# Optimization experiments

Measured on AMD Instinct MI355X. Metric: run time of the kernel, lower is better.

Reference implementation:

```python
import jax, jax.numpy as jnp
import numpy as np

N = 25000      # nodes
E = 300000     # edges
IN = 32        # in_dim
EDF = 16       # edge_feat_dim
HID = 256      # hidden_dim (per-head dim, concat=False)
HEADS = 4
ACT = 16       # num_actions
G = 64         # graphs in batch
KW = 1024      # wire-mask query nodes


def setup_inputs() -> dict:
    key = jax.random.key(0)
    ks = jax.random.split(key, 20)
    def rn(k, shape, s=0.1):
        return jax.random.normal(k, shape, jnp.float32) * s
    return {
        "x": jax.random.normal(ks[0], (N, IN), jnp.float32),
        "edge_attr": jax.random.normal(ks[1], (E, EDF), jnp.float32),
        "wire_mask": jax.random.randint(ks[2], (KW,), 0, N, jnp.int32),
        "edge_index": jax.random.randint(ks[3], (2, E), 0, N, jnp.int32),
        "batch": jnp.sort(jax.random.randint(ks[4], (N,), 0, G, jnp.int32)),
        "enc_w1": rn(ks[5], (EDF, 32)),
        "enc_b1": jnp.zeros((32,), jnp.float32),
        "enc_w2": rn(ks[6], (32, IN * IN), 0.05),
        "enc_b2": jnp.zeros((IN * IN,), jnp.float32),
        "root_w": rn(ks[7], (IN, IN)),
        "nn_bias": jnp.zeros((IN,), jnp.float32),
        "gat1_w": rn(ks[8], (IN, HEADS * HID)),
        "gat1_asrc": rn(ks[9], (HEADS, HID)),
        "gat1_adst": rn(ks[10], (HEADS, HID)),
        "gat1_b": jnp.zeros((HID,), jnp.float32),
        "gat2_w": rn(ks[11], (HID, HEADS * HID)),
        "gat2_asrc": rn(ks[12], (HEADS, HID)),
        "gat2_adst": rn(ks[13], (HEADS, HID)),
        "gat2_b": jnp.zeros((HID,), jnp.float32),
        "wire_w": rn(ks[14], (HID, 1)),
        "wire_b": jnp.zeros((1,), jnp.float32),
        "act_w": rn(ks[15], (HID, ACT)),
        "act_b": jnp.zeros((ACT,), jnp.float32),
    }


def _gat(x, src, dst, W, a_src, a_dst, b):
    # PyG GATConv, concat=False (mean over heads), eval mode (no dropout),
    # self-loops already included in (src, dst).
    H, D = a_src.shape
    h = (x @ W).reshape(-1, H, D)                      # [N, H, D]
    es = (h * a_src[None]).sum(-1)                     # [N, H]
    ed = (h * a_dst[None]).sum(-1)                     # [N, H]
    e = jax.nn.leaky_relu(es[src] + ed[dst], negative_slope=0.2)  # [E2, H]
    m = jax.ops.segment_max(e, dst, num_segments=N)    # segment softmax (stable)
    w = jnp.exp(e - m[dst])
    den = jax.ops.segment_sum(w, dst, num_segments=N)
    alpha = w / (den[dst] + 1e-16)
    out = jax.ops.segment_sum(h[src] * alpha[..., None], dst, num_segments=N)
    return out.mean(axis=1) + b                        # [N, D]


def reference(x, edge_attr, wire_mask, edge_index, batch,
              enc_w1, enc_b1, enc_w2, enc_b2, root_w, nn_bias,
              gat1_w, gat1_asrc, gat1_adst, gat1_b,
              gat2_w, gat2_asrc, gat2_adst, gat2_b,
              wire_w, wire_b, act_w, act_b):
    src, dst = edge_index[0], edge_index[1]
    # NNConv (aggr='mean'): per-edge weight matrix from edge MLP
    We = (jax.nn.relu(edge_attr @ enc_w1 + enc_b1) @ enc_w2 + enc_b2)
    We = We.reshape(E, IN, IN)                         # [E, in, out]
    msg = jnp.einsum('ei,eio->eo', x[src], We)         # [E, out]
    s = jax.ops.segment_sum(msg, dst, num_segments=N)
    cnt = jax.ops.segment_sum(jnp.ones((E,), x.dtype), dst, num_segments=N)
    agg = s / jnp.maximum(cnt, 1.0)[:, None]
    h0 = jax.nn.relu(agg + x @ root_w + nn_bias)
    # GATConv default add_self_loops=True
    sl = jnp.arange(N, dtype=src.dtype)
    src2 = jnp.concatenate([src, sl])
    dst2 = jnp.concatenate([dst, sl])
    h1 = jax.nn.relu(_gat(h0, src2, dst2, gat1_w, gat1_asrc, gat1_adst, gat1_b))
    h2 = jax.nn.relu(_gat(h1, src2, dst2, gat2_w, gat2_asrc, gat2_adst, gat2_b))
    p_wire = (h2[wire_mask] @ wire_w + wire_b).squeeze(-1)   # [KW]
    pooled_s = jax.ops.segment_sum(h2, batch, num_segments=G)
    gc = jax.ops.segment_sum(jnp.ones((N,), h2.dtype), batch, num_segments=G)
    pooled = pooled_s / jnp.maximum(gc, 1.0)[:, None]        # global_mean_pool
    p_action = pooled @ act_w + act_b                        # [G, ACT]
    return (p_wire, p_action)
```

## Files before the change

### kernel.cpp

```cpp
#include <hip/hip_runtime.h>
#include <hip/hip_fp16.h>

#define N_NODES 25000
#define M_PAD   25024
#define N_TILES 1564
#define N_EDGES 300000
#define IN_DIM  32
#define EDFD    16
#define HIDD    256
#define HEADS   4
#define NACT    16
#define NGRAPH  64
#define KWIRE   1024
#define POOL_NB 64

typedef _Float16 half8v __attribute__((ext_vector_type(8)));
typedef __attribute__((ext_vector_type(4))) float f32x4;

__device__ __forceinline__ float leaky(float v) { return v > 0.f ? v : 0.2f * v; }

__global__ __launch_bounds__(256) void k_deg2(const int* __restrict__ ei,
                                              int* __restrict__ deg,
                                              int* __restrict__ deg2) {
    int e = blockIdx.x * 256 + threadIdx.x;
    if (e >= N_EDGES) return;
    atomicAdd(&deg[ei[N_EDGES + e]], 1);
    atomicAdd(&deg2[ei[e]], 1);
}

__global__ __launch_bounds__(256) void k_scan2(const int* __restrict__ degA, int* __restrict__ rpA,
                                               const int* __restrict__ degB, int* __restrict__ rpB) {
    const int* deg = blockIdx.x ? degB : degA;
    int* rowptr    = blockIdx.x ? rpB : rpA;
    __shared__ int part[256];
    int t = threadIdx.x;
    const int CH = 98;
    int base = t * CH;
    int s = 0;
    for (int i = 0; i < CH; ++i) {
        int idx = base + i;
        if (idx < N_NODES) s += deg[idx];
    }
    part[t] = s;
    __syncthreads();
    if (t == 0) {
        int run = 0;
        for (int i = 0; i < 256; ++i) { int v = part[i]; part[i] = run; run += v; }
    }
    __syncthreads();
    int run = part[t];
    for (int i = 0; i < CH; ++i) {
        int idx = base + i;
        if (idx < N_NODES) { rowptr[idx] = run; run += deg[idx]; }
    }
    if (N_NODES >= base && N_NODES < base + CH) rowptr[N_NODES] = run;
}

__global__ __launch_bounds__(256) void k_scatter2(const int* __restrict__ ei,
                                                  const float* __restrict__ ea,
                                                  const int* __restrict__ rowptr,
                                                  const int* __restrict__ rowptr2,
                                                  int* __restrict__ cursor,
                                                  int* __restrict__ cursor2,
                                                  int* __restrict__ csrc,
                                                  int* __restrict__ cdst,
                                                  int* __restrict__ posMap,
                                                  __half* __restrict__ eaP) {
    int e = blockIdx.x * 256 + threadIdx.x;
    if (e >= N_EDGES) return;
    int src = ei[e], dst = ei[N_EDGES + e];
    int p1 = atomicAdd(&cursor[dst], 1);
    int r1 = rowptr[dst] + p1;
    csrc[r1] = src;
    int p2 = atomicAdd(&cursor2[src], 1);
    int r2 = rowptr2[src] + p2;
    cdst[r2] = dst;
    posMap[r2] = r1;
    const float4* src4 = (const float4*)(ea + (size_t)e * EDFD);
    __half2* dp = (__half2*)(eaP + (size_t)r2 * EDFD);
    #pragma unroll
    for (int q = 0; q < EDFD / 4; ++q) {
        float4 v = src4[q];
        dp[q * 2]     = __float22half2_rn(make_float2(v.x, v.y));
        dp[q * 2 + 1] = __float22half2_rn(make_float2(v.z, v.w));
    }
}

__global__ __launch_bounds__(256) void k_prep(const float* __restrict__ w2,
                                              const float* __restrict__ W1,
                                              const float* __restrict__ W2,
                                              const float* __restrict__ a1s,
                                              const float* __restrict__ a1d,
                                              const float* __restrict__ a2s,
                                              const float* __restrict__ a2d,
                                              const float* __restrict__ x,
                                              const float* __restrict__ b2,
                                              __half* __restrict__ wtt,
                                              __half* __restrict__ wb1,
                                              __half* __restrict__ wb2,
                                              float* __restrict__ wa1,
                                              float* __restrict__ wd1,
                                              float* __restrict__ wa2,
                                              float* __restrict__ wd2,
                                              __half* __restrict__ xf,
                                              float* __restrict__ xb) {
    int bid = blockIdx.x, t = threadIdx.x;
    if (bid < 128) {
        int idx = bid * 256 + t;
        int co = idx >> 5, i = idx & 31;
        wtt[idx] = __float2half(w2[(co >> 5) * 1024 + i * 32 + (co & 31)]);
    } else if (bid < 256) {
        int idx = (bid - 128) * 256 + t;
        int d = idx >> 7, k = idx & 127;
        int h = k >> 5, i = k & 31;
        wb1[idx] = __float2half(0.25f * W1[i * 1024 + h * 256 + d]);
    } else if (bid < 1280) {
        int idx = (bid - 256) * 256 + t;
        int d = idx >> 10, k = idx & 1023;
        int h = k >> 8, i = k & 255;
        wb2[idx] = __float2half(0.25f * W2[i * 1024 + h * 256 + d]);
    } else if (bid < 4405) {
        int idx = (bid - 1280) * 256 + t;
        if (idx >= N_NODES * 32) return;
        int n = idx >> 5, o = idx & 31;
        xf[idx] = __float2half(x[idx]);
        float s = 0.f;
        for (int i = 0; i < 32; ++i) s += x[n * 32 + i] * b2[i * 32 + o];
        xb[idx] = s;
    } else if (bid == 4405) {
        if (t >= 128) return;
        int h = t >> 5, i = t & 31;
        float s = 0.f, sd = 0.f;
        for (int d = 0; d < 256; ++d) {
            float w = W1[i * 1024 + h * 256 + d];
            s  += w * a1s[h * 256 + d];
            sd += w * a1d[h * 256 + d];
        }
        wa1[t] = s; wd1[t] = sd;
    } else {
        int idx = (bid - 4406) * 256 + t;
        if (idx >= 1024) return;
        int h = idx >> 8, i = idx & 255;
        float s = 0.f, sd = 0.f;
        for (int d = 0; d < 256; ++d) {
            float w = W2[i * 1024 + h * 256 + d];
            s  += w * a2s[h * 256 + d];
            sd += w * a2d[h * 256 + d];
        }
        wa2[idx] = s; wd2[idx] = sd;
    }
}

__global__ __launch_bounds__(256) void k_msg2(const int* __restrict__ rowptr2,
                                              const int* __restrict__ posMap,
                                              const __half* __restrict__ eaP,
                                              const float* __restrict__ w1,
                                              const float* __restrict__ b1,
                                              const __half* __restrict__ T,
                                              const float* __restrict__ xb,
                                              __half* __restrict__ msgE) {
    int g = threadIdx.x >> 5, o = threadIdx.x & 31;
    int src = blockIdx.x * 8 + g;
    if (src >= N_NODES) return;
    int r0 = rowptr2[src], r1 = rowptr2[src + 1];
    if (r0 == r1) return;
    float tcol[32];
    const __half* Tp = T + (size_t)src * 1024 + o;
    #pragma unroll
    for (int j = 0; j < 32; ++j) tcol[j] = __half2float(Tp[j * 32]);
    float w1col[EDFD];
    #pragma unroll
    for (int k = 0; k < EDFD; ++k) w1col[k] = w1[k * 32 + o];
    float b1o = b1[o];
    float xbv = xb[src * 32 + o];
    for (int r = r0; r < r1; ++r) {
        int pm = posMap[r];
        const __half2* h2p = (const __half2*)(eaP + (size_t)r * EDFD);
        float a = b1o;
        #pragma unroll
        for (int q = 0; q < EDFD / 2; ++q) {
            float2 v = __half22float2(h2p[q]);
            a += v.x * w1col[2 * q] + v.y * w1col[2 * q + 1];
        }
        a = fmaxf(a, 0.f);
        float m0 = 0.f, m1 = 0.f, m2 = 0.f, m3 = 0.f;
        #pragma unroll
        for (int j = 0; j < 32; j += 4) {
            m0 += __shfl(a, j,     32) * tcol[j];
            m1 += __shfl(a, j + 1, 32) * tcol[j + 1];
            m2 += __shfl(a, j + 2, 32) * tcol[j + 2];
            m3 += __shfl(a, j + 3, 32) * tcol[j + 3];
        }
        float m = xbv + ((m0 + m1) + (m2 + m3));
        msgE[(size_t)pm * 32 + o] = __float2half(m);
    }
}

__global__ __launch_bounds__(256) void k_h0e(const float* __restrict__ x,
                                             const float* __restrict__ root_w,
                                             const float* __restrict__ nn_bias,
                                             const __half* __restrict__ msgE,
                                             const int* __restrict__ rowptr,
                                             const float* __restrict__ wa,
                                             const float* __restrict__ wd,
                                             __half* __restrict__ h0f,
                                             float* __restrict__ es,
                                             float* __restrict__ ed) {
    int t = threadIdx.x;
    int ng = t >> 5, o = t & 31;
    int n = blockIdx.x * 8 + ng;
    if (n >= N_NODES) return;
    float s = nn_bias[o];
    for (int k = 0; k < IN_DIM; ++k) s += x[n * IN_DIM + k] * root_w[k * 32 + o];
    int r0 = rowptr[n], r1 = rowptr[n + 1];
    float aggv = 0.f;
    for (int r = r0; r < r1; ++r)
        aggv += __half2float(msgE[(size_t)r * 32 + o]);
    float c = fmaxf((float)(r1 - r0), 1.f);
    s += aggv / c;
    float v = fmaxf(s, 0.f);
    h0f[n * IN_DIM + o] = __float2half(v);
    #pragma unroll
    for (int h = 0; h < 4; ++h) {
        float ss = v * wa[h * 32 + o];
        float dd = v * wd[h * 32 + o];
        #pragma unroll
        for (int off = 16; off; off >>= 1) {
            ss += __shfl_down(ss, off, 32);
            dd += __shfl_down(dd, off, 32);
        }
        if (o == 0) { es[n * 4 + h] = ss; ed[n * 4 + h] = dd; }
    }
}

__global__ __launch_bounds__(256, 2) void k_gemT(const __half* __restrict__ A,
                                                 const __half* __restrict__ Wt,
                                                 __half* __restrict__ C) {
    __shared__ __half cst[4][16 * 36];
    int t = threadIdx.x, wid = t >> 6, lane = t & 63;
    int lr = lane & 15, lk = (lane >> 4) * 8;

    int bid = blockIdx.x;
    int xcd = bid & 7, j = bid >> 3;
    int sx = j & 31;
    int y = ((j >> 5) << 3) | xcd;
    int n0 = sx * 32;

    half8v bfr[2];
    #pragma unroll
    for (int c = 0; c < 2; ++c)
        bfr[c] = *(const half8v*)(Wt + (size_t)(n0 + c * 16 + lr) * 32 + lk);

    int tb = (y * 4 + wid) * 4;
    for (int pp = 0; pp < 4; pp += 2) {
        int tA = tb + pp;
        if (tA >= N_TILES) break;
        int mA = tA * 16, mB = mA + 16;
        half8v aA = *(const half8v*)(A + (size_t)(mA + lr) * 32 + lk);
        half8v aB = *(const half8v*)(A + (size_t)(mB + lr) * 32 + lk);
        f32x4 acc[2][2];
        #pragma unroll
        for (int i = 0; i < 2; ++i)
            #pragma unroll
            for (int c = 0; c < 2; ++c)
                acc[i][c] = (f32x4){0.f, 0.f, 0.f, 0.f};
        acc[0][0] = __builtin_amdgcn_mfma_f32_16x16x32_f16(aA, bfr[0], acc[0][0], 0, 0, 0);
        acc[0][1] = __builtin_amdgcn_mfma_f32_16x16x32_f16(aA, bfr[1], acc[0][1], 0, 0, 0);
        acc[1][0] = __builtin_amdgcn_mfma_f32_16x16x32_f16(aB, bfr[0], acc[1][0], 0, 0, 0);
        acc[1][1] = __builtin_amdgcn_mfma_f32_16x16x32_f16(aB, bfr[1], acc[1][1], 0, 0, 0);

        int rbase = (lane >> 4) * 4;
        #pragma unroll
        for (int ti = 0; ti < 2; ++ti) {
            #pragma unroll
            for (int c = 0; c < 2; ++c)
                #pragma unroll
                for (int r = 0; r < 4; ++r)
                    cst[wid][(rbase + r) * 36 + c * 16 + lr] = __float2half(acc[ti][c][r]);
            int m0 = ti ? mB : mA;
            #pragma unroll
            for (int p = 0; p < 2; ++p) {
                int row = p * 8 + (lane >> 3), hb = lane & 7;
                float2 v = *(const float2*)((const char*)&cst[wid][0] + row * 72 + hb * 8);
                *(float2*)((char*)C + ((size_t)(m0 + row) * 1024 + n0) * 2 + hb * 8) = v;
            }
        }
    }
}

template <int K, typename OT>
__global__ __launch_bounds__(256) void k_gemmo(const __half* __restrict__ A,
                                               const __half* __restrict__ Wt,
                                               const float* __restrict__ bias,
                                               OT* __restrict__ C) {
    constexpr int CK  = 128;
    constexpr int KC  = K / CK;
    constexpr int KSC = CK / 32;
    constexpr int CB  = CK * 2;
    __shared__ __half bs[2][32 * CK];
    __shared__ float cst[4][16 * 36];
    int t = threadIdx.x, wid = t >> 6, lane = t & 63;
    int lr = lane & 15, lk = (lane >> 4) * 8;

    int bid = blockIdx.x;
    int xcd = bid & 7, rest = bid >> 3;
    int strip = rest & 7, yhi = rest >> 3;
    int y = yhi * 8 + xcd;
    if (y >= 98) return;
    int n0 = strip * 32;
    float bv0 = bias[n0 + lr], bv1 = bias[n0 + 16 + lr];
    int tb = (y * 4 + wid) * 4;
    const int swz = (lr & 7) << 4;

    f32x4 acc[2][2][2];
    #pragma unroll
    for (int pi = 0; pi < 2; ++pi)
        #pragma unroll
        for (int i = 0; i < 2; ++i)
            #pragma unroll
            for (int c = 0; c < 2; ++c)
                acc[pi][i][c] = (f32x4){0.f, 0.f, 0.f, 0.f};

    for (int i = t * 16; i < 32 * CB; i += 256 * 16) {
        int col = i / CB, offb = i % CB;
        const char* src = (const char*)Wt + ((size_t)(n0 + col) * K) * 2 + offb;
        *(float4*)((char*)bs[0] + (i ^ ((col & 7) << 4))) = *(const float4*)src;
    }
    __syncthreads();

    for (int kc = 0; kc < KC; ++kc) {
        int cur = kc & 1;
        if (kc + 1 < KC) {
            for (int i = t * 16; i < 32 * CB; i += 256 * 16) {
                int col = i / CB, offb = i % CB;
                const char* src = (const char*)Wt + (((size_t)(n0 + col) * K + (kc + 1) * CK) * 2 + offb);
                *(float4*)((char*)bs[cur ^ 1] + (i ^ ((col & 7) << 4))) = *(const float4*)src;
            }
        }
        #pragma unroll
        for (int pi = 0; pi < 2; ++pi) {
            int tA = tb + pi * 2;
            if (tA >= N_TILES) continue;
            int mA = tA * 16, mB = mA + 16;
            const __half* pA = A + (size_t)(mA + lr) * K + kc * CK + lk;
            const __half* pB = A + (size_t)(mB + lr) * K + kc * CK + lk;
            #pragma unroll
            for (int ks = 0; ks < KSC; ++ks) {
                half8v aA = *(const half8v*)(pA + (size_t)ks * 32);
                half8v aB = *(const half8v*)(pB + (size_t)ks * 32);
                half8v b0 = *(const half8v*)((const char*)bs[cur] + ((( 0 + lr) * CB + lk * 2 + ks * 64) ^ swz));
                half8v b1 = *(const half8v*)((const char*)bs[cur] + (((16 + lr) * CB + lk * 2 + ks * 64) ^ swz));
                acc[pi][0][0] = __builtin_amdgcn_mfma_f32_16x16x32_f16(aA, b0, acc[pi][0][0], 0, 0, 0);
                acc[pi][0][1] = __builtin_amdgcn_mfma_f32_16x16x32_f16(aA, b1, acc[pi][0][1], 0, 0, 0);
                acc[pi][1][0] = __builtin_amdgcn_mfma_f32_16x16x32_f16(aB, b0, acc[pi][1][0], 0, 0, 0);
                acc[pi][1][1] = __builtin_amdgcn_mfma_f32_16x16x32_f16(aB, b1, acc[pi][1][1], 0, 0, 0);
            }
        }
        if (kc + 1 < KC) __syncthreads();
    }

    int rbase = (lane >> 4) * 4;
    #pragma unroll
    for (int pi = 0; pi < 2; ++pi) {
        int tA = tb + pi * 2;
        if (tA >= N_TILES) continue;
        #pragma unroll
        for (int ti = 0; ti < 2; ++ti) {
            #pragma unroll
            for (int c = 0; c < 2; ++c)
                #pragma unroll
                for (int r = 0; r < 4; ++r)
                    cst[wid][(rbase + r) * 36 + c * 16 + lr] =
                        fmaxf(acc[pi][ti][c][r] + (c ? bv1 : bv0), 0.f);
            int m0 = tA * 16 + ti * 16;
            int row = lane >> 2, cg = lane & 3;
            const float* sp = &cst[wid][row * 36 + cg * 8];
            if constexpr (sizeof(OT) == 2) {
                __half2 o0 = __float22half2_rn(make_float2(sp[0], sp[1]));
                __half2 o1 = __float22half2_rn(make_float2(sp[2], sp[3]));
                __half2 o2 = __float22half2_rn(make_float2(sp[4], sp[5]));
                __half2 o3 = __float22half2_rn(make_float2(sp[6], sp[7]));
                float4 v = make_float4(__uint_as_float(*(unsigned*)&o0), __uint_as_float(*(unsigned*)&o1),
                                       __uint_as_float(*(unsigned*)&o2), __uint_as_float(*(unsigned*)&o3));
                *(float4*)((__half*)C + (size_t)(m0 + row) * 256 + n0 + cg * 8) = v;
            } else {
                float4 v0 = make_float4(sp[0], sp[1], sp[2], sp[3]);
                float4 v1 = make_float4(sp[4], sp[5], sp[6], sp[7]);
                float* cp = (float*)C + (size_t)(m0 + row) * 256 + n0 + cg * 8;
                *(float4*)cp = v0;
                *(float4*)(cp + 4) = v1;
            }
        }
    }
}

__global__ __launch_bounds__(256) void k_esed2(const __half* __restrict__ h1f,
                                               const float* __restrict__ wa,
                                               const float* __restrict__ wd,
                                               float* __restrict__ es,
                                               float* __restrict__ ed) {
    int n = blockIdx.x;
    int h = threadIdx.x >> 6, lane = threadIdx.x & 63;
    float s = 0.f, d2 = 0.f;
    for (int d = lane; d < 256; d += 64) {
        float v = __half2float(h1f[(size_t)n * 256 + d]);
        s  += v * wa[h * 256 + d];
        d2 += v * wd[h * 256 + d];
    }
    #pragma unroll
    for (int off = 32; off; off >>= 1) {
        s  += __shfl_down(s, off);
        d2 += __shfl_down(d2, off);
    }
    if (lane == 0) { es[n * 4 + h] = s; ed[n * 4 + h] = d2; }
}

__global__ __launch_bounds__(256) void k_agg1(const int* __restrict__ rowptr,
                                              const int* __restrict__ csrc,
                                              const float* __restrict__ es,
                                              const float* __restrict__ ed,
                                              const __half* __restrict__ h0f,
                                              __half* __restrict__ agg0) {
    int dst = blockIdx.x * 4 + (threadIdx.x >> 6);
    if (dst >= N_NODES) return;
    int lane = threadIdx.x & 63;
    int h = lane >> 4, i2 = lane & 15;
    float edv = ed[dst * 4 + h];
    float vself = leaky(es[dst * 4 + h] + edv);
    float dn = 1.f;
    int r0 = rowptr[dst], r1 = rowptr[dst + 1];

    __half2 hv = *(const __half2*)(h0f + (size_t)dst * 32 + i2 * 2);
    float2 f = __half22float2(hv);
    float ax = f.x, ay = f.y;
    for (int r = r0; r < r1; ++r) {
        int src = csrc[r];
        float w = __expf(leaky(es[src * 4 + h] + edv) - vself);
        dn += w;
        __half2 sv = *(const __half2*)(h0f + (size_t)src * 32 + i2 * 2);
        float2 g = __half22float2(sv);
        ax += w * g.x; ay += w * g.y;
    }
    float inv = 1.f / (dn + 1e-16f);
    *(__half2*)(agg0 + (size_t)dst * 128 + h * 32 + i2 * 2) =
        __float22half2_rn(make_float2(ax * inv, ay * inv));
}

__global__ __launch_bounds__(256) void k_agg2(const int* __restrict__ rowptr,
                                              const int* __restrict__ csrc,
                                              const float* __restrict__ es,
                                              const float* __restrict__ ed,
                                              const __half* __restrict__ h1f,
                                              __half* __restrict__ agg1) {
    int dst = blockIdx.x * 4 + (threadIdx.x >> 6);
    if (dst >= N_NODES) return;
    int lane = threadIdx.x & 63;
    float vs[4], edv[4], dn[4];
    float acc[4][4];
    {
        float2 q = *(const float2*)(h1f + (size_t)dst * 256 + lane * 4);
        const __half2* hq = (const __half2*)&q;
        float2 f0 = __half22float2(hq[0]), f1 = __half22float2(hq[1]);
        #pragma unroll
        for (int h = 0; h < 4; ++h) {
            edv[h] = ed[dst * 4 + h];
            vs[h] = leaky(es[dst * 4 + h] + edv[h]);
            dn[h] = 1.f;
            acc[h][0] = f0.x; acc[h][1] = f0.y;
            acc[h][2] = f1.x; acc[h][3] = f1.y;
        }
    }
    int r0 = rowptr[dst], r1 = rowptr[dst + 1];
    for (int r = r0; r < r1; ++r) {
        int src = csrc[r];
        float4 esv = *(const float4*)(es + (size_t)src * 4);
        float w0 = __expf(leaky(esv.x + edv[0]) - vs[0]);
        float w1 = __expf(leaky(esv.y + edv[1]) - vs[1]);
        float w2 = __expf(leaky(esv.z + edv[2]) - vs[2]);
        float w3 = __expf(leaky(esv.w + edv[3]) - vs[3]);
        dn[0] += w0; dn[1] += w1; dn[2] += w2; dn[3] += w3;
        float2 q = *(const float2*)(h1f + (size_t)src * 256 + lane * 4);
        const __half2* hq = (const __half2*)&q;
        float2 f0 = __half22float2(hq[0]), f1 = __half22float2(hq[1]);
        acc[0][0] += w0 * f0.x; acc[0][1] += w0 * f0.y; acc[0][2] += w0 * f1.x; acc[0][3] += w0 * f1.y;
        acc[1][0] += w1 * f0.x; acc[1][1] += w1 * f0.y; acc[1][2] += w1 * f1.x; acc[1][3] += w1 * f1.y;
        acc[2][0] += w2 * f0.x; acc[2][1] += w2 * f0.y; acc[2][2] += w2 * f1.x; acc[2][3] += w2 * f1.y;
        acc[3][0] += w3 * f0.x; acc[3][1] += w3 * f0.y; acc[3][2] += w3 * f1.x; acc[3][3] += w3 * f1.y;
    }
    #pragma unroll
    for (int h = 0; h < 4; ++h) {
        float inv = 1.f / (dn[h] + 1e-16f);
        __half2 o0 = __float22half2_rn(make_float2(acc[h][0] * inv, acc[h][1] * inv));
        __half2 o1 = __float22half2_rn(make_float2(acc[h][2] * inv, acc[h][3] * inv));
        __half2* op = (__half2*)(agg1 + (size_t)dst * 1024 + h * 256 + lane * 4);
        op[0] = o0; op[1] = o1;
    }
}

__global__ __launch_bounds__(256) void k_wirepool(const int* __restrict__ wm,
                                                  const float* __restrict__ h2,
                                                  const float* __restrict__ ww,
                                                  const float* __restrict__ wb,
                                                  const int* __restrict__ batch,
                                                  float* __restrict__ out,
                                                  float* __restrict__ pooled,
                                                  float* __restrict__ gcnt) {
    int bid = blockIdx.x;
    if (bid < KWIRE / 4) {
        int k = bid * 4 + (threadIdx.x >> 6);
        int lane = threadIdx.x & 63;
        int n = wm[k];
        float s = 0.f;
        for (int d = lane; d < 256; d += 64) s += h2[(size_t)n * 256 + d] * ww[d];
        #pragma unroll
        for (int off = 32; off; off >>= 1) s += __shfl_down(s, off);
        if (lane == 0) out[k] = s + wb[0];
        return;
    }
    int n0 = (bid - KWIRE / 4) * POOL_NB;
    int n1 = n0 + POOL_NB; if (n1 > N_NODES) n1 = N_NODES;
    int d = threadIdx.x;
    int cur = batch[n0];
    float acc = 0.f, cnt = 0.f;
    for (int n = n0; n < n1; ++n) {
        int g = batch[n];
        if (g != cur) {
            atomicAdd(&pooled[cur * 256 + d], acc);
            if (d == 0) atomicAdd(&gcnt[cur], cnt);
            acc = 0.f; cnt = 0.f; cur = g;
        }
        acc += h2[(size_t)n * 256 + d];
        cnt += 1.f;
    }
    atomicAdd(&pooled[cur * 256 + d], acc);
    if (d == 0) atomicAdd(&gcnt[cur], cnt);
}

__global__ __launch_bounds__(256) void k_act(const float* __restrict__ pooled,
                                             const float* __restrict__ gcnt,
                                             const float* __restrict__ aw,
                                             const float* __restrict__ ab,
                                             float* __restrict__ out) {
    int u = blockIdx.x * 4 + (threadIdx.x >> 6);
    int lane = threadIdx.x & 63;
    if (u >= NGRAPH * NACT) return;
    int g = u >> 4, a = u & 15;
    float c = fmaxf(gcnt[g], 1.f);
    float s = 0.f;
    for (int d = lane; d < 256; d += 64) s += pooled[g * 256 + d] * aw[d * 16 + a];
    #pragma unroll
    for (int off = 32; off; off >>= 1) s += __shfl_down(s, off);
    if (lane == 0) out[KWIRE + u] = s / c + ab[a];
}

extern "C" void kernel_launch(void* const* d_in, const int* in_sizes, int n_in,
                              void* d_out, int out_size, void* d_ws, size_t ws_size,
                              hipStream_t stream) {
    const float* x        = (const float*)d_in[0];
    const float* edge_attr= (const float*)d_in[1];
    const int*   wire_mask= (const int*)d_in[2];
    const int*   edge_idx = (const int*)d_in[3];
    const int*   batch    = (const int*)d_in[4];
    const float* enc_w1   = (const float*)d_in[5];
    const float* enc_b1   = (const float*)d_in[6];
    const float* enc_w2   = (const float*)d_in[7];
    const float* enc_b2   = (const float*)d_in[8];
    const float* root_w   = (const float*)d_in[9];
    const float* nn_bias  = (const float*)d_in[10];
    const float* gat1_w   = (const float*)d_in[11];
    const float* gat1_asrc= (const float*)d_in[12];
    const float* gat1_adst= (const float*)d_in[13];
    const float* gat1_b   = (const float*)d_in[14];
    const float* gat2_w   = (const float*)d_in[15];
    const float* gat2_asrc= (const float*)d_in[16];
    const float* gat2_adst= (const float*)d_in[17];
    const float* gat2_b   = (const float*)d_in[18];
    const float* wire_w   = (const float*)d_in[19];
    const float* wire_b   = (const float*)d_in[20];
    const float* act_w    = (const float*)d_in[21];
    const float* act_b    = (const float*)d_in[22];
    float* out = (float*)d_out;

    float* ws = (float*)d_ws;
    size_t off = 0;
    __half* T16   = (__half*)(ws + off); off += (size_t)M_PAD * 1024 / 2;
    __half* agg1f = (__half*)(ws + off); off += (size_t)M_PAD * 1024 / 2;
    __half* agg0f = (__half*)(ws + off); off += (size_t)M_PAD * 128 / 2;
    __half* h0f   = (__half*)(ws + off); off += (size_t)M_PAD * 32 / 2;
    __half* h1f   = (__half*)(ws + off); off += (size_t)M_PAD * 256 / 2;
    __half* xf    = (__half*)(ws + off); off += (size_t)M_PAD * 32 / 2;
    __half* eaP   = (__half*)(ws + off); off += (size_t)N_EDGES * EDFD / 2;
    __half* msgE  = (__half*)(ws + off); off += (size_t)N_EDGES * 32 / 2;
    float* xb     = ws + off; off += 800000;
    float* esb    = ws + off; off += 100000;
    float* edb    = ws + off; off += 100000;
    float* h2     = ws + off; off += (size_t)M_PAD * 256;
    float* pooled = ws + off; off += NGRAPH * 256;
    float* gcnt   = ws + off; off += NGRAPH;
    int* deg      = (int*)(ws + off); off += 25600;
    int* deg2     = (int*)(ws + off); off += 25600;
    int* cursor   = (int*)(ws + off); off += 25600;
    int* cursor2  = (int*)(ws + off); off += 25600;
    int* rowptr   = (int*)(ws + off); off += 25600;
    int* rowptr2  = (int*)(ws + off); off += 25600;
    int* csrc     = (int*)(ws + off); off += N_EDGES;
    int* cdst     = (int*)(ws + off); off += N_EDGES;
    int* posMap   = (int*)(ws + off); off += N_EDGES;
    __half* wtt   = (__half*)(ws + off); off += 16384;
    __half* wb1t  = (__half*)(ws + off); off += 16384;
    __half* wb2t  = (__half*)(ws + off); off += 131072;
    float* wa1    = ws + off; off += 128;
    float* wd1    = ws + off; off += 128;
    float* wa2    = ws + off; off += 1024;
    float* wd2    = ws + off; off += 1024;

    const int GBT = 3328;
    const int GBO = 832;

    hipMemsetAsync(deg, 0, 4 * 25600 * sizeof(int), stream);
    k_deg2<<<(N_EDGES + 255) / 256, 256, 0, stream>>>(edge_idx, deg, deg2);
    k_scan2<<<2, 256, 0, stream>>>(deg, rowptr, deg2, rowptr2);
    k_scatter2<<<(N_EDGES + 255) / 256, 256, 0, stream>>>(edge_idx, edge_attr, rowptr, rowptr2,
                                                          cursor, cursor2, csrc, cdst, posMap, eaP);

    k_prep<<<4410, 256, 0, stream>>>(enc_w2, gat1_w, gat2_w, gat1_asrc, gat1_adst,
                                     gat2_asrc, gat2_adst, x, enc_b2,
                                     wtt, wb1t, wb2t, wa1, wd1, wa2, wd2, xf, xb);

    k_gemT<<<GBT, 256, 0, stream>>>(xf, wtt, T16);
    k_msg2<<<(N_NODES + 7) / 8, 256, 0, stream>>>(rowptr2, posMap, eaP,
                                                  enc_w1, enc_b1, T16, xb, msgE);
    k_h0e<<<(N_NODES + 7) / 8, 256, 0, stream>>>(x, root_w, nn_bias, msgE, rowptr,
                                                 wa1, wd1, h0f, esb, edb);

    k_agg1<<<(N_NODES + 3) / 4, 256, 0, stream>>>(rowptr, csrc, esb, edb, h0f, agg0f);
    k_gemmo<128, __half><<<GBO, 256, 0, stream>>>(agg0f, wb1t, gat1_b, h1f);
    k_esed2<<<N_NODES, 256, 0, stream>>>(h1f, wa2, wd2, esb, edb);

    k_agg2<<<(N_NODES + 3) / 4, 256, 0, stream>>>(rowptr, csrc, esb, edb, h1f, agg1f);
    k_gemmo<1024, float><<<GBO, 256, 0, stream>>>(agg1f, wb2t, gat2_b, h2);

    hipMemsetAsync(pooled, 0, (NGRAPH * 256 + NGRAPH) * sizeof(float), stream);
    k_wirepool<<<KWIRE / 4 + (N_NODES + POOL_NB - 1) / POOL_NB, 256, 0, stream>>>(
        wire_mask, h2, wire_w, wire_b, batch, out, pooled, gcnt);
    k_act<<<NGRAPH * NACT / 4, 256, 0, stream>>>(pooled, gcnt, act_w, act_b, out);
}
```

Measured before the change: 453.5 us.

## Compute per-source edge messages with MFMA tiles instead of shuffle dot products

```diff
diff --git a/kernel.cpp b/kernel.cpp
--- a/kernel.cpp
+++ b/kernel.cpp
@@ -95,6 +95,7 @@
                                               const float* __restrict__ a2d,
                                               const float* __restrict__ x,
                                               const float* __restrict__ b2,
+                                              const float* __restrict__ w1,
                                               __half* __restrict__ wtt,
                                               __half* __restrict__ wb1,
                                               __half* __restrict__ wb2,
@@ -103,7 +104,8 @@
                                               float* __restrict__ wa2,
                                               float* __restrict__ wd2,
                                               __half* __restrict__ xf,
-                                              float* __restrict__ xb) {
+                                              float* __restrict__ xb,
+                                              __half* __restrict__ w1t) {
     int bid = blockIdx.x, t = threadIdx.x;
     if (bid < 128) {
         int idx = bid * 256 + t;
@@ -137,7 +139,7 @@
             sd += w * a1d[h * 256 + d];
         }
         wa1[t] = s; wd1[t] = sd;
-    } else {
+    } else if (bid < 4410) {
         int idx = (bid - 4406) * 256 + t;
         if (idx >= 1024) return;
         int h = idx >> 8, i = idx & 255;
@@ -148,51 +150,87 @@
             sd += w * a2d[h * 256 + d];
         }
         wa2[idx] = s; wd2[idx] = sd;
-    }
-}
-
-__global__ __launch_bounds__(256) void k_msg2(const int* __restrict__ rowptr2,
+    } else {
+        int idx = (bid - 4410) * 256 + t;
+        if (idx >= 32 * EDFD) return;
+        int j = idx >> 4, k = idx & 15;
+        w1t[idx] = __float2half(w1[k * 32 + j]);
+    }
+}
+
+__global__ __launch_bounds__(256) void k_msg3(const int* __restrict__ rowptr2,
                                               const int* __restrict__ posMap,
                                               const __half* __restrict__ eaP,
-                                              const float* __restrict__ w1,
+                                              const __half* __restrict__ w1t,
                                               const float* __restrict__ b1,
                                               const __half* __restrict__ T,
                                               const float* __restrict__ xb,
                                               __half* __restrict__ msgE) {
-    int g = threadIdx.x >> 5, o = threadIdx.x & 31;
-    int src = blockIdx.x * 8 + g;
+    int wv = threadIdx.x >> 6, lane = threadIdx.x & 63;
+    int src = blockIdx.x * 4 + wv;
     if (src >= N_NODES) return;
     int r0 = rowptr2[src], r1 = rowptr2[src + 1];
     if (r0 == r1) return;
-    float tcol[32];
-    const __half* Tp = T + (size_t)src * 1024 + o;
-    #pragma unroll
-    for (int j = 0; j < 32; ++j) tcol[j] = __half2float(Tp[j * 32]);
-    float w1col[EDFD];
-    #pragma unroll
-    for (int k = 0; k < EDFD; ++k) w1col[k] = w1[k * 32 + o];
-    float b1o = b1[o];
-    float xbv = xb[src * 32 + o];
-    for (int r = r0; r < r1; ++r) {
-        int pm = posMap[r];
-        const __half2* h2p = (const __half2*)(eaP + (size_t)r * EDFD);
-        float a = b1o;
-        #pragma unroll
-        for (int q = 0; q < EDFD / 2; ++q) {
-            float2 v = __half22float2(h2p[q]);
-            a += v.x * w1col[2 * q] + v.y * w1col[2 * q + 1];
-        }
-        a = fmaxf(a, 0.f);
-        float m0 = 0.f, m1 = 0.f, m2 = 0.f, m3 = 0.f;
-        #pragma unroll
-        for (int j = 0; j < 32; j += 4) {
-            m0 += __shfl(a, j,     32) * tcol[j];
-            m1 += __shfl(a, j + 1, 32) * tcol[j + 1];
-            m2 += __shfl(a, j + 2, 32) * tcol[j + 2];
-            m3 += __shfl(a, j + 3, 32) * tcol[j + 3];
-        }
-        float m = xbv + ((m0 + m1) + (m2 + m3));
-        msgE[(size_t)pm * 32 + o] = __float2half(m);
+    int lr = lane & 15, lk = (lane >> 4) * 8;
+
+    half8v bf0, bf1;
+    const __half* Tp = T + (size_t)src * 1024;
+    #pragma unroll
+    for (int q = 0; q < 8; ++q) {
+        bf0[q] = (_Float16)__half2float(Tp[(lk + q) * 32 + lr]);
+        bf1[q] = (_Float16)__half2float(Tp[(lk + q) * 32 + 16 + lr]);
+    }
+
+    __half2 w1r[8][EDFD / 2];
+    #pragma unroll
+    for (int q = 0; q < 8; ++q) {
+        const __half2* wp = (const __half2*)(w1t + (lk + q) * EDFD);
+        #pragma unroll
+        for (int k2 = 0; k2 < EDFD / 2; ++k2) w1r[q][k2] = wp[k2];
+    }
+    float b1r[8];
+    #pragma unroll
+    for (int q = 0; q < 8; ++q) b1r[q] = b1[lk + q];
+
+    float xb0 = xb[src * 32 + lr], xb1 = xb[src * 32 + 16 + lr];
+    int rbase = (lane >> 4) * 4;
+
+    for (int t0 = r0; t0 < r1; t0 += 16) {
+        int e = t0 + lr;
+        bool ok = (e < r1);
+        half8v afr;
+        if (ok) {
+            const __half2* ep = (const __half2*)(eaP + (size_t)e * EDFD);
+            __half2 ea2[EDFD / 2];
+            #pragma unroll
+            for (int k2 = 0; k2 < EDFD / 2; ++k2) ea2[k2] = ep[k2];
+            #pragma unroll
+            for (int q = 0; q < 8; ++q) {
+                float s = b1r[q];
+                #pragma unroll
+                for (int k2 = 0; k2 < EDFD / 2; ++k2) {
+                    float2 v = __half22float2(ea2[k2]);
+                    float2 w = __half22float2(w1r[q][k2]);
+                    s += v.x * w.x + v.y * w.y;
+                }
+                afr[q] = (_Float16)fmaxf(s, 0.f);
+            }
+        } else {
+            #pragma unroll
+            for (int q = 0; q < 8; ++q) afr[q] = (_Float16)0.f;
+        }
+        f32x4 c0 = {0.f, 0.f, 0.f, 0.f}, c1 = {0.f, 0.f, 0.f, 0.f};
+        c0 = __builtin_amdgcn_mfma_f32_16x16x32_f16(afr, bf0, c0, 0, 0, 0);
+        c1 = __builtin_amdgcn_mfma_f32_16x16x32_f16(afr, bf1, c1, 0, 0, 0);
+        #pragma unroll
+        for (int r = 0; r < 4; ++r) {
+            int er = t0 + rbase + r;
+            if (er < r1) {
+                int pm = posMap[er];
+                msgE[(size_t)pm * 32 + lr]      = __float2half(c0[r] + xb0);
+                msgE[(size_t)pm * 32 + 16 + lr] = __float2half(c1[r] + xb1);
+            }
+        }
     }
 }
 
@@ -609,6 +647,7 @@
     __half* wtt   = (__half*)(ws + off); off += 16384;
     __half* wb1t  = (__half*)(ws + off); off += 16384;
     __half* wb2t  = (__half*)(ws + off); off += 131072;
+    __half* w1t   = (__half*)(ws + off); off += 256;
     float* wa1    = ws + off; off += 128;
     float* wd1    = ws + off; off += 128;
     float* wa2    = ws + off; off += 1024;
@@ -623,13 +662,13 @@
     k_scatter2<<<(N_EDGES + 255) / 256, 256, 0, stream>>>(edge_idx, edge_attr, rowptr, rowptr2,
                                                           cursor, cursor2, csrc, cdst, posMap, eaP);
 
-    k_prep<<<4410, 256, 0, stream>>>(enc_w2, gat1_w, gat2_w, gat1_asrc, gat1_adst,
-                                     gat2_asrc, gat2_adst, x, enc_b2,
-                                     wtt, wb1t, wb2t, wa1, wd1, wa2, wd2, xf, xb);
+    k_prep<<<4412, 256, 0, stream>>>(enc_w2, gat1_w, gat2_w, gat1_asrc, gat1_adst,
+                                     gat2_asrc, gat2_adst, x, enc_b2, enc_w1,
+                                     wtt, wb1t, wb2t, wa1, wd1, wa2, wd2, xf, xb, w1t);
 
     k_gemT<<<GBT, 256, 0, stream>>>(xf, wtt, T16);
-    k_msg2<<<(N_NODES + 7) / 8, 256, 0, stream>>>(rowptr2, posMap, eaP,
-                                                  enc_w1, enc_b1, T16, xb, msgE);
+    k_msg3<<<(N_NODES + 3) / 4, 256, 0, stream>>>(rowptr2, posMap, eaP,
+                                                  w1t, enc_b1, T16, xb, msgE);
     k_h0e<<<(N_NODES + 7) / 8, 256, 0, stream>>>(x, root_w, nn_bias, msgE, rowptr,
                                                  wa1, wd1, h0f, esb, edb);
 
```

New measurement: 430.3 us. 1.05x faster.
